# Performance work log

Hardware: AMD Instinct MI355X
Metric: run time of the kernel (lower is better)

## Reference

```python
import jax, jax.numpy as jnp
import numpy as np

INPUT_SIZE = 2048
HIDDEN_SIZE = 2048
BATCH = 4096


def setup_inputs() -> dict:
    key = jax.random.key(0)
    ks = jax.random.split(key, 24)
    s_in = 1.0 / np.sqrt(INPUT_SIZE)
    s_h = 1.0 / np.sqrt(HIDDEN_SIZE)
    inp = {
        "x": jax.random.normal(ks[0], (BATCH, INPUT_SIZE), jnp.float32),
        "h_prev": jax.random.normal(ks[1], (BATCH, HIDDEN_SIZE), jnp.float32),
        "c_prev": jax.random.normal(ks[2], (BATCH, HIDDEN_SIZE), jnp.float32),
        "n_prev": jnp.ones((BATCH, HIDDEN_SIZE), jnp.float32),
        "m_prev": jnp.zeros((BATCH, HIDDEN_SIZE), jnp.float32),
    }
    # 4 input projections (W*x) and 4 recurrent projections (R*h), each Linear w/ bias.
    names_x = ["Wzx", "Wix", "Wfx", "Wox"]
    names_h = ["Rzh", "Rih", "Rfh", "Roh"]
    for j, n in enumerate(names_x):
        inp[n + "_w"] = jax.random.uniform(ks[3 + 2 * j], (HIDDEN_SIZE, INPUT_SIZE), jnp.float32, -s_in, s_in)
        inp[n + "_b"] = jax.random.uniform(ks[4 + 2 * j], (HIDDEN_SIZE,), jnp.float32, -s_in, s_in)
    for j, n in enumerate(names_h):
        inp[n + "_w"] = jax.random.uniform(ks[11 + 2 * j], (HIDDEN_SIZE, HIDDEN_SIZE), jnp.float32, -s_h, s_h)
        inp[n + "_b"] = jax.random.uniform(ks[12 + 2 * j], (HIDDEN_SIZE,), jnp.float32, -s_h, s_h)
    return inp


def _lin(x, w, b):
    return x @ w.T + b


def reference(x, h_prev, c_prev, n_prev, m_prev,
              Wzx_w, Wzx_b, Wix_w, Wix_b, Wfx_w, Wfx_b, Wox_w, Wox_b,
              Rzh_w, Rzh_b, Rih_w, Rih_b, Rfh_w, Rfh_b, Roh_w, Roh_b):
    z = jnp.tanh(_lin(x, Wzx_w, Wzx_b) + _lin(h_prev, Rzh_w, Rzh_b))
    # log(i) and log(f) are the pre-activations (i = exp(pre_i), f = exp(pre_f))
    log_i = _lin(x, Wix_w, Wix_b) + _lin(h_prev, Rih_w, Rih_b)
    log_f = _lin(x, Wfx_w, Wfx_b) + _lin(h_prev, Rfh_w, Rfh_b)
    o = jax.nn.sigmoid(_lin(x, Wox_w, Wox_b) + _lin(h_prev, Roh_w, Roh_b))
    m = jnp.maximum(log_f + m_prev, log_i)  # stabilizer state
    i_hat = jnp.exp(log_i - m)
    f_hat = jnp.exp(log_f + m_prev - m)
    c = f_hat * c_prev + i_hat * z
    n = f_hat * n_prev + i_hat
    h = o * c / n
    return (h, c, n, m)
```

## Files before the change

kernel.cpp:

```cpp
#include <hip/hip_runtime.h>
#include <hip/hip_bf16.h>


#define BATCH 4096
#define NHID  2048
#define KDIM  4096
#define NTOT  8388608L
#define AW_OFS 16777216

typedef float  f32x4   __attribute__((ext_vector_type(4)));
typedef short  short8  __attribute__((ext_vector_type(8)));
typedef unsigned short ushort8 __attribute__((ext_vector_type(8)));

#define GL_LDS16(gp, lp)                                                      \
    __builtin_amdgcn_global_load_lds(                                         \
        (const __attribute__((address_space(1))) void*)(gp),                  \
        (__attribute__((address_space(3))) void*)(lp), 16, 0, 0)

__device__ __forceinline__ unsigned short f2bf(float f) {
    unsigned u = __float_as_uint(f);
    unsigned r = (u + 0x7fffu + ((u >> 16) & 1u)) >> 16;
    return (unsigned short)r;
}

__global__ void convA_kernel(const float* __restrict__ x,
                             const float* __restrict__ h,
                             unsigned short* __restrict__ A) {
    int gid = blockIdx.x * 256 + threadIdx.x;
    int row = gid >> 9;
    int col = (gid & 511) << 3;
    const float* src = (col < 2048) ? (x + (long)row * 2048 + col)
                                    : (h + (long)row * 2048 + (col - 2048));
    f32x4 v0 = __builtin_nontemporal_load((const f32x4*)src);
    f32x4 v1 = __builtin_nontemporal_load((const f32x4*)src + 1);
    ushort8 o;
    o[0] = f2bf(v0[0]); o[1] = f2bf(v0[1]); o[2] = f2bf(v0[2]); o[3] = f2bf(v0[3]);
    o[4] = f2bf(v1[0]); o[5] = f2bf(v1[1]); o[6] = f2bf(v1[2]); o[7] = f2bf(v1[3]);
    *(ushort8*)(A + ((long)row << 12) + col) = o;
}

__global__ void convW_kernel(const float* __restrict__ w0, const float* __restrict__ w1,
                             const float* __restrict__ w2, const float* __restrict__ w3,
                             const float* __restrict__ w4, const float* __restrict__ w5,
                             const float* __restrict__ w6, const float* __restrict__ w7,
                             unsigned short* __restrict__ Wb) {
    int z = blockIdx.y;
    const float* src;
    switch (z) {
        case 0: src = w0; break; case 1: src = w1; break;
        case 2: src = w2; break; case 3: src = w3; break;
        case 4: src = w4; break; case 5: src = w5; break;
        case 6: src = w6; break; default: src = w7; break;
    }
    int gid = blockIdx.x * 256 + threadIdx.x;
    int row = gid >> 8;
    int col = (gid & 255) << 3;
    const float* p = src + (long)row * 2048 + col;
    f32x4 v0 = __builtin_nontemporal_load((const f32x4*)p);
    f32x4 v1 = __builtin_nontemporal_load((const f32x4*)p + 1);
    ushort8 o;
    o[0] = f2bf(v0[0]); o[1] = f2bf(v0[1]); o[2] = f2bf(v0[2]); o[3] = f2bf(v0[3]);
    o[4] = f2bf(v1[0]); o[5] = f2bf(v1[1]); o[6] = f2bf(v1[2]); o[7] = f2bf(v1[3]);
    int g = z & 3, hf = z >> 2;
    *(ushort8*)(Wb + (long)g * NHID * KDIM + (long)row * KDIM + hf * 2048 + col) = o;
}

__global__ void bias_kernel(const float* __restrict__ b0, const float* __restrict__ b1,
                            const float* __restrict__ b2, const float* __restrict__ b3,
                            const float* __restrict__ r0, const float* __restrict__ r1,
                            const float* __restrict__ r2, const float* __restrict__ r3,
                            float* __restrict__ Bb) {
    int gid = blockIdx.x * 256 + threadIdx.x;
    int g = gid >> 11, j = gid & 2047;
    const float *wb, *rb;
    switch (g) {
        case 0: wb = b0; rb = r0; break; case 1: wb = b1; rb = r1; break;
        case 2: wb = b2; rb = r2; break; default: wb = b3; rb = r3; break;
    }
    Bb[gid] = wb[j] + rb[j];
}

__global__ __launch_bounds__(512, 4) void slstm_kernel(
    const __hip_bfloat16* __restrict__ A,
    const float* __restrict__ Bb,
    const float* __restrict__ c_prev,
    const float* __restrict__ n_prev,
    const float* __restrict__ m_prev,
    float* __restrict__ out)
{
    __shared__ uint4 smem4[49152 / 16];
    char* smem = (char*)smem4;

    const int tid  = threadIdx.x;
    const int lane = tid & 63;
    const int wv   = tid >> 6;
    const int gate = wv & 3;
    const int rh   = wv >> 2;
    const int lm   = lane & 15;
    const int quad = lane >> 4;
    const int l7   = lm & 7;

    const int row0 = blockIdx.x * 128;
    const int col0 = blockIdx.y * 64;

    int gofs[6]; char* lds[6];
#pragma unroll
    for (int t = 0; t < 6; ++t) {
        int id = wv * 6 + t;
        if (id < 16) {
            int idx = id * 64 + lane;
            int r = idx >> 3, jj = idx & 7;
            int j = jj ^ (r & 7);
            gofs[t] = (row0 + r) * KDIM + j * 8;
            lds[t]  = smem + id * 1024;
        } else {
            int idx = (id - 16) * 64 + lane;
            int g = idx >> 9, rr = (idx >> 3) & 63, jj = idx & 7;
            int j = jj ^ (rr & 7);
            gofs[t] = AW_OFS + (g * NHID + col0 + rr) * KDIM + j * 8;
            lds[t]  = smem + 16384 + (id - 16) * 1024;
        }
    }

    f32x4 acc[4][4];
#pragma unroll
    for (int mt = 0; mt < 4; ++mt)
#pragma unroll
        for (int nt = 0; nt < 4; ++nt)
#pragma unroll
            for (int r = 0; r < 4; ++r) acc[mt][nt][r] = 0.0f;

    const char* aB = smem + rh * 8192;
    const char* bB = smem + 16384 + gate * 8192;

    for (int kt = 0; kt < KDIM / 64; ++kt) {
        const int k0 = kt * 64;
        __syncthreads();
#pragma unroll
        for (int t = 0; t < 6; ++t) GL_LDS16(A + gofs[t] + k0, lds[t]);
        __syncthreads();
#pragma unroll
        for (int kk = 0; kk < 2; ++kk) {
            const int cof = ((kk * 4 + quad) ^ l7) * 16;
            short8 af[4], bf[4];
#pragma unroll
            for (int mt = 0; mt < 4; ++mt)
                af[mt] = *(const short8*)(aB + (mt * 16 + lm) * 128 + cof);
#pragma unroll
            for (int nt = 0; nt < 4; ++nt)
                bf[nt] = *(const short8*)(bB + (nt * 16 + lm) * 128 + cof);
#pragma unroll
            for (int mt = 0; mt < 4; ++mt)
#pragma unroll
                for (int nt = 0; nt < 4; ++nt)
                    acc[mt][nt] = __builtin_amdgcn_mfma_f32_16x16x32_bf16(
                        af[mt], bf[nt], acc[mt][nt], 0, 0, 0);
        }
    }

    float* exch = (float*)smem;
#pragma unroll
    for (int mt = 0; mt < 4; ++mt) {
        __syncthreads();
#pragma unroll
        for (int nt = 0; nt < 4; ++nt)
#pragma unroll
            for (int r = 0; r < 4; ++r)
                exch[((rh * 4 + gate) * 16 + quad * 4 + r) * 65 + nt * 16 + lm] =
                    acc[mt][nt][r];
        __syncthreads();
#pragma unroll
        for (int q = 0; q < 4; ++q) {
            int e   = q * 512 + tid;
            int erh = e >> 10, row = (e >> 6) & 15, col = e & 63;
            int R = row0 + erh * 64 + mt * 16 + row;
            int C = col0 + col;
            long idx = (long)R * NHID + C;
            float zp = exch[((erh * 4 + 0) * 16 + row) * 65 + col] + Bb[C];
            float ip = exch[((erh * 4 + 1) * 16 + row) * 65 + col] + Bb[2048 + C];
            float fp = exch[((erh * 4 + 2) * 16 + row) * 65 + col] + Bb[4096 + C];
            float op = exch[((erh * 4 + 3) * 16 + row) * 65 + col] + Bb[6144 + C];
            float cp = __builtin_nontemporal_load(c_prev + idx);
            float np = __builtin_nontemporal_load(n_prev + idx);
            float mp = __builtin_nontemporal_load(m_prev + idx);
            float z  = tanhf(zp);
            float o  = 1.0f / (1.0f + __expf(-op));
            float mm = fmaxf(fp + mp, ip);
            float ih = __expf(ip - mm);
            float fh = __expf(fp + mp - mm);
            float cc = fh * cp + ih * z;
            float nn = fh * np + ih;
            float hh = o * cc / nn;
            __builtin_nontemporal_store(hh, out + idx);
            __builtin_nontemporal_store(cc, out + NTOT + idx);
            __builtin_nontemporal_store(nn, out + 2 * NTOT + idx);
            __builtin_nontemporal_store(mm, out + 3 * NTOT + idx);
        }
    }
}

extern "C" void kernel_launch(void* const* d_in, const int* in_sizes, int n_in,
                              void* d_out, int out_size, void* d_ws, size_t ws_size,
                              hipStream_t stream) {
    const float* x      = (const float*)d_in[0];
    const float* h_prev = (const float*)d_in[1];
    const float* c_prev = (const float*)d_in[2];
    const float* n_prev = (const float*)d_in[3];
    const float* m_prev = (const float*)d_in[4];
    unsigned short* A  = (unsigned short*)d_ws;
    unsigned short* Wb = (unsigned short*)((char*)d_ws + 33554432);
    float*          Bb = (float*)((char*)d_ws + 100663296);

    convA_kernel<<<8192, 256, 0, stream>>>(x, h_prev, A);
    convW_kernel<<<dim3(2048, 8), 256, 0, stream>>>(
        (const float*)d_in[5], (const float*)d_in[7], (const float*)d_in[9],
        (const float*)d_in[11], (const float*)d_in[13], (const float*)d_in[15],
        (const float*)d_in[17], (const float*)d_in[19], Wb);
    bias_kernel<<<32, 256, 0, stream>>>(
        (const float*)d_in[6], (const float*)d_in[8], (const float*)d_in[10],
        (const float*)d_in[12], (const float*)d_in[14], (const float*)d_in[16],
        (const float*)d_in[18], (const float*)d_in[20], Bb);

    slstm_kernel<<<dim3(32, 32), 512, 0, stream>>>(
        (const __hip_bfloat16*)A, Bb, c_prev, n_prev, m_prev, (float*)d_out);
}
```

Before: 583.9 us.

## Pre-pack operands into k-chunk-major layout and switch to 32x32x16 MFMA

The conversion kernels now stage through shared memory and write A and W in a k-chunk-major packed layout (8 bf16 per chunk, rows contiguous). The GEMM loads straight from that layout into LDS without XOR swizzling and uses 32x32x16 bf16 MFMA with a 2x2 accumulator tile per wave instead of 4x4 16x16 tiles. It also raises wave priority around the MFMA section. The aim is to cut LDS read instructions and address arithmetic per MFMA. The unswizzled LDS layout may add bank conflicts, and the transpose adds an extra sync to the conversion kernels.

```diff
diff --git a/kernel.cpp b/kernel.cpp
--- a/kernel.cpp
+++ b/kernel.cpp
@@ -9,6 +9,7 @@
 #define AW_OFS 16777216
 
 typedef float  f32x4   __attribute__((ext_vector_type(4)));
+typedef float  f32x16  __attribute__((ext_vector_type(16)));
 typedef short  short8  __attribute__((ext_vector_type(8)));
 typedef unsigned short ushort8 __attribute__((ext_vector_type(8)));
 
@@ -25,26 +26,35 @@
 
 __global__ void convA_kernel(const float* __restrict__ x,
                              const float* __restrict__ h,
-                             unsigned short* __restrict__ A) {
-    int gid = blockIdx.x * 256 + threadIdx.x;
-    int row = gid >> 9;
-    int col = (gid & 511) << 3;
-    const float* src = (col < 2048) ? (x + (long)row * 2048 + col)
-                                    : (h + (long)row * 2048 + (col - 2048));
+                             unsigned short* __restrict__ Ap) {
+    __shared__ unsigned short tile[8][32][8];
+    const int t  = threadIdx.x;
+    const int r  = t >> 3, c8 = t & 7;
+    const int row = blockIdx.x * 32 + r;
+    const int k0  = blockIdx.y * 64;
+    const float* src = (blockIdx.y < 32)
+        ? (x + (long)row * 2048 + k0 + c8 * 8)
+        : (h + (long)row * 2048 + (k0 - 2048) + c8 * 8);
     f32x4 v0 = __builtin_nontemporal_load((const f32x4*)src);
     f32x4 v1 = __builtin_nontemporal_load((const f32x4*)src + 1);
     ushort8 o;
     o[0] = f2bf(v0[0]); o[1] = f2bf(v0[1]); o[2] = f2bf(v0[2]); o[3] = f2bf(v0[3]);
     o[4] = f2bf(v1[0]); o[5] = f2bf(v1[1]); o[6] = f2bf(v1[2]); o[7] = f2bf(v1[3]);
-    *(ushort8*)(A + ((long)row << 12) + col) = o;
+    *(ushort8*)&tile[c8][(r ^ (c8 << 2)) & 31][0] = o;
+    __syncthreads();
+    const int kcl = t >> 5, rr = t & 31;
+    ushort8 w = *(ushort8*)&tile[kcl][(rr ^ (kcl << 2)) & 31][0];
+    long dst = ((long)(blockIdx.y * 8 + kcl) * 4096 + blockIdx.x * 32 + rr) * 8;
+    __builtin_nontemporal_store(w, (ushort8*)(Ap + dst));
 }
 
 __global__ void convW_kernel(const float* __restrict__ w0, const float* __restrict__ w1,
                              const float* __restrict__ w2, const float* __restrict__ w3,
                              const float* __restrict__ w4, const float* __restrict__ w5,
                              const float* __restrict__ w6, const float* __restrict__ w7,
-                             unsigned short* __restrict__ Wb) {
-    int z = blockIdx.y;
+                             unsigned short* __restrict__ Wp) {
+    __shared__ unsigned short tile[8][32][8];
+    const int z = blockIdx.z;
     const float* src;
     switch (z) {
         case 0: src = w0; break; case 1: src = w1; break;
@@ -52,17 +62,24 @@
         case 4: src = w4; break; case 5: src = w5; break;
         case 6: src = w6; break; default: src = w7; break;
     }
-    int gid = blockIdx.x * 256 + threadIdx.x;
-    int row = gid >> 8;
-    int col = (gid & 255) << 3;
-    const float* p = src + (long)row * 2048 + col;
+    const int g = z & 3, hf = z >> 2;
+    const int t = threadIdx.x;
+    const int r = t >> 3, c8 = t & 7;
+    const int j  = blockIdx.x * 32 + r;
+    const int k2 = blockIdx.y * 64 + c8 * 8;
+    const float* p = src + (long)j * 2048 + k2;
     f32x4 v0 = __builtin_nontemporal_load((const f32x4*)p);
     f32x4 v1 = __builtin_nontemporal_load((const f32x4*)p + 1);
     ushort8 o;
     o[0] = f2bf(v0[0]); o[1] = f2bf(v0[1]); o[2] = f2bf(v0[2]); o[3] = f2bf(v0[3]);
     o[4] = f2bf(v1[0]); o[5] = f2bf(v1[1]); o[6] = f2bf(v1[2]); o[7] = f2bf(v1[3]);
-    int g = z & 3, hf = z >> 2;
-    *(ushort8*)(Wb + (long)g * NHID * KDIM + (long)row * KDIM + hf * 2048 + col) = o;
+    *(ushort8*)&tile[c8][(r ^ (c8 << 2)) & 31][0] = o;
+    __syncthreads();
+    const int kcl = t >> 5, rr = t & 31;
+    ushort8 w = *(ushort8*)&tile[kcl][(rr ^ (kcl << 2)) & 31][0];
+    const int kcg = hf * 256 + blockIdx.y * 8 + kcl;
+    long dst = ((long)kcg * 8192 + g * 2048 + blockIdx.x * 32 + rr) * 8;
+    __builtin_nontemporal_store(w, (ushort8*)(Wp + dst));
 }
 
 __global__ void bias_kernel(const float* __restrict__ b0, const float* __restrict__ b1,
@@ -81,7 +98,7 @@
 }
 
 __global__ __launch_bounds__(512, 4) void slstm_kernel(
-    const __hip_bfloat16* __restrict__ A,
+    const unsigned short* __restrict__ Ap,
     const float* __restrict__ Bb,
     const float* __restrict__ c_prev,
     const float* __restrict__ n_prev,
@@ -96,90 +113,90 @@
     const int wv   = tid >> 6;
     const int gate = wv & 3;
     const int rh   = wv >> 2;
-    const int lm   = lane & 15;
-    const int quad = lane >> 4;
-    const int l7   = lm & 7;
+    const int l31  = lane & 31;
+    const int lhi  = lane >> 5;
 
     const int row0 = blockIdx.x * 128;
     const int col0 = blockIdx.y * 64;
 
-    int gofs[6]; char* lds[6];
+    const int abase = lhi * 2048 + (rh * 64 + l31) * 16;
+    const int bbase = 16384 + lhi * 4096 + (gate * 64 + l31) * 16;
+
+    int gofs[6], strd[6], lofs[6];
 #pragma unroll
     for (int t = 0; t < 6; ++t) {
         int id = wv * 6 + t;
+        lofs[t] = id * 1024 + lane * 16;
         if (id < 16) {
             int idx = id * 64 + lane;
-            int r = idx >> 3, jj = idx & 7;
-            int j = jj ^ (r & 7);
-            gofs[t] = (row0 + r) * KDIM + j * 8;
-            lds[t]  = smem + id * 1024;
+            int kc = idx >> 7, row = idx & 127;
+            gofs[t] = (kc * 4096 + row0 + row) * 8;
+            strd[t] = 8 * 4096 * 8;
         } else {
             int idx = (id - 16) * 64 + lane;
-            int g = idx >> 9, rr = (idx >> 3) & 63, jj = idx & 7;
-            int j = jj ^ (rr & 7);
-            gofs[t] = AW_OFS + (g * NHID + col0 + rr) * KDIM + j * 8;
-            lds[t]  = smem + 16384 + (id - 16) * 1024;
-        }
-    }
-
-    f32x4 acc[4][4];
-#pragma unroll
-    for (int mt = 0; mt < 4; ++mt)
-#pragma unroll
-        for (int nt = 0; nt < 4; ++nt)
-#pragma unroll
-            for (int r = 0; r < 4; ++r) acc[mt][nt][r] = 0.0f;
-
-    const char* aB = smem + rh * 8192;
-    const char* bB = smem + 16384 + gate * 8192;
-
-    for (int kt = 0; kt < KDIM / 64; ++kt) {
-        const int k0 = kt * 64;
-        __syncthreads();
-#pragma unroll
-        for (int t = 0; t < 6; ++t) GL_LDS16(A + gofs[t] + k0, lds[t]);
-        __syncthreads();
-#pragma unroll
-        for (int kk = 0; kk < 2; ++kk) {
-            const int cof = ((kk * 4 + quad) ^ l7) * 16;
-            short8 af[4], bf[4];
-#pragma unroll
-            for (int mt = 0; mt < 4; ++mt)
-                af[mt] = *(const short8*)(aB + (mt * 16 + lm) * 128 + cof);
-#pragma unroll
-            for (int nt = 0; nt < 4; ++nt)
-                bf[nt] = *(const short8*)(bB + (nt * 16 + lm) * 128 + cof);
-#pragma unroll
-            for (int mt = 0; mt < 4; ++mt)
-#pragma unroll
-                for (int nt = 0; nt < 4; ++nt)
-                    acc[mt][nt] = __builtin_amdgcn_mfma_f32_16x16x32_bf16(
-                        af[mt], bf[nt], acc[mt][nt], 0, 0, 0);
-        }
+            int kc = idx >> 8, gr = idx & 255;
+            gofs[t] = AW_OFS + (kc * 8192 + (gr >> 6) * 2048 + col0 + (gr & 63)) * 8;
+            strd[t] = 8 * 8192 * 8;
+        }
+    }
+
+    f32x16 acc[2][2];
+#pragma unroll
+    for (int mt = 0; mt < 2; ++mt)
+#pragma unroll
+        for (int nt = 0; nt < 2; ++nt)
+#pragma unroll
+            for (int r = 0; r < 16; ++r) acc[mt][nt][r] = 0.0f;
+
+    for (int kt = 0; kt < 64; ++kt) {
+        __syncthreads();
+#pragma unroll
+        for (int t = 0; t < 6; ++t) {
+            GL_LDS16(Ap + gofs[t], smem + lofs[t]);
+            gofs[t] += strd[t];
+        }
+        __syncthreads();
+
+        __builtin_amdgcn_s_setprio(1);
+#pragma unroll
+        for (int ks = 0; ks < 4; ++ks) {
+            short8 a0 = *(const short8*)(smem + abase + ks * 4096);
+            short8 a1 = *(const short8*)(smem + abase + ks * 4096 + 512);
+            short8 b0 = *(const short8*)(smem + bbase + ks * 8192);
+            short8 b1 = *(const short8*)(smem + bbase + ks * 8192 + 512);
+            acc[0][0] = __builtin_amdgcn_mfma_f32_32x32x16_bf16(a0, b0, acc[0][0], 0, 0, 0);
+            acc[0][1] = __builtin_amdgcn_mfma_f32_32x32x16_bf16(a0, b1, acc[0][1], 0, 0, 0);
+            acc[1][0] = __builtin_amdgcn_mfma_f32_32x32x16_bf16(a1, b0, acc[1][0], 0, 0, 0);
+            acc[1][1] = __builtin_amdgcn_mfma_f32_32x32x16_bf16(a1, b1, acc[1][1], 0, 0, 0);
+        }
+        __builtin_amdgcn_s_setprio(0);
     }
 
     float* exch = (float*)smem;
 #pragma unroll
-    for (int mt = 0; mt < 4; ++mt) {
-        __syncthreads();
-#pragma unroll
-        for (int nt = 0; nt < 4; ++nt)
-#pragma unroll
-            for (int r = 0; r < 4; ++r)
-                exch[((rh * 4 + gate) * 16 + quad * 4 + r) * 65 + nt * 16 + lm] =
-                    acc[mt][nt][r];
+    for (int s = 0; s < 4; ++s) {
+        __syncthreads();
+        if (rh == (s >> 1)) {
+#pragma unroll
+            for (int nt = 0; nt < 2; ++nt)
+#pragma unroll
+                for (int r = 0; r < 16; ++r) {
+                    int lrow = (r & 3) + 8 * (r >> 2) + 4 * lhi;
+                    exch[(gate * 32 + lrow) * 65 + nt * 32 + l31] = acc[s & 1][nt][r];
+                }
+        }
         __syncthreads();
 #pragma unroll
         for (int q = 0; q < 4; ++q) {
             int e   = q * 512 + tid;
-            int erh = e >> 10, row = (e >> 6) & 15, col = e & 63;
-            int R = row0 + erh * 64 + mt * 16 + row;
+            int row = e >> 6, col = e & 63;
+            int R = row0 + s * 32 + row;
             int C = col0 + col;
             long idx = (long)R * NHID + C;
-            float zp = exch[((erh * 4 + 0) * 16 + row) * 65 + col] + Bb[C];
-            float ip = exch[((erh * 4 + 1) * 16 + row) * 65 + col] + Bb[2048 + C];
-            float fp = exch[((erh * 4 + 2) * 16 + row) * 65 + col] + Bb[4096 + C];
-            float op = exch[((erh * 4 + 3) * 16 + row) * 65 + col] + Bb[6144 + C];
+            float zp = exch[(0 * 32 + row) * 65 + col] + Bb[C];
+            float ip = exch[(1 * 32 + row) * 65 + col] + Bb[2048 + C];
+            float fp = exch[(2 * 32 + row) * 65 + col] + Bb[4096 + C];
+            float op = exch[(3 * 32 + row) * 65 + col] + Bb[6144 + C];
             float cp = __builtin_nontemporal_load(c_prev + idx);
             float np = __builtin_nontemporal_load(n_prev + idx);
             float mp = __builtin_nontemporal_load(m_prev + idx);
@@ -207,20 +224,20 @@
     const float* c_prev = (const float*)d_in[2];
     const float* n_prev = (const float*)d_in[3];
     const float* m_prev = (const float*)d_in[4];
-    unsigned short* A  = (unsigned short*)d_ws;
-    unsigned short* Wb = (unsigned short*)((char*)d_ws + 33554432);
+    unsigned short* Ap = (unsigned short*)d_ws;
+    unsigned short* Wp = (unsigned short*)((char*)d_ws + 33554432);
     float*          Bb = (float*)((char*)d_ws + 100663296);
 
-    convA_kernel<<<8192, 256, 0, stream>>>(x, h_prev, A);
-    convW_kernel<<<dim3(2048, 8), 256, 0, stream>>>(
+    convA_kernel<<<dim3(128, 64), 256, 0, stream>>>(x, h_prev, Ap);
+    convW_kernel<<<dim3(64, 32, 8), 256, 0, stream>>>(
         (const float*)d_in[5], (const float*)d_in[7], (const float*)d_in[9],
         (const float*)d_in[11], (const float*)d_in[13], (const float*)d_in[15],
-        (const float*)d_in[17], (const float*)d_in[19], Wb);
+        (const float*)d_in[17], (const float*)d_in[19], Wp);
     bias_kernel<<<32, 256, 0, stream>>>(
         (const float*)d_in[6], (const float*)d_in[8], (const float*)d_in[10],
         (const float*)d_in[12], (const float*)d_in[14], (const float*)d_in[16],
         (const float*)d_in[18], (const float*)d_in[20], Bb);
 
     slstm_kernel<<<dim3(32, 32), 512, 0, stream>>>(
-        (const __hip_bfloat16*)A, Bb, c_prev, n_prev, m_prev, (float*)d_out);
-}
+        Ap, Bb, c_prev, n_prev, m_prev, (float*)d_out);
+}
```

Measured after the change: 623.8 us. 1.07x slower.

## Double-buffer LDS tiles with K=32 steps to overlap global loads with MFMA

Applied to the files above, without the earlier changes.

Replaces the single-buffered K=64 main loop with a two-buffer K=32 pipeline. The next tile's global-to-LDS loads are issued before the current tile's MFMAs, so memory latency is hidden behind compute. Each iteration needs one waitcnt plus barrier instead of two syncthreads. The swizzle is reworked for 64-byte rows. The trade-offs are twice as many iterations, each with less work per barrier, and a vmcnt(0) wait that fully drains loads every step.

```diff
diff --git a/kernel.cpp b/kernel.cpp
--- a/kernel.cpp
+++ b/kernel.cpp
@@ -7,6 +7,7 @@
 #define KDIM  4096
 #define NTOT  8388608L
 #define AW_OFS 16777216
+#define BUFSZ 24576
 
 typedef float  f32x4   __attribute__((ext_vector_type(4)));
 typedef short  short8  __attribute__((ext_vector_type(8)));
@@ -88,7 +89,7 @@
     const float* __restrict__ m_prev,
     float* __restrict__ out)
 {
-    __shared__ uint4 smem4[49152 / 16];
+    __shared__ uint4 smem4[(2 * BUFSZ) / 16];
     char* smem = (char*)smem4;
 
     const int tid  = threadIdx.x;
@@ -98,27 +99,31 @@
     const int rh   = wv >> 2;
     const int lm   = lane & 15;
     const int quad = lane >> 4;
-    const int l7   = lm & 7;
 
     const int row0 = blockIdx.x * 128;
     const int col0 = blockIdx.y * 64;
 
-    int gofs[6]; char* lds[6];
-#pragma unroll
-    for (int t = 0; t < 6; ++t) {
-        int id = wv * 6 + t;
-        if (id < 16) {
+    const int cof   = ((quad ^ (lm & 3))) * 16;
+    const int abase = (rh * 64 + lm) * 64 + cof;
+    const int bbase = 8192 + (gate * 64 + lm) * 64 + cof;
+
+    int gofs[3], lofs[3];
+#pragma unroll
+    for (int t = 0; t < 3; ++t) {
+        int id = wv * 3 + t;
+        if (id < 8) {
             int idx = id * 64 + lane;
-            int r = idx >> 3, jj = idx & 7;
-            int j = jj ^ (r & 7);
+            int r = idx >> 2, jj = idx & 3;
+            int j = jj ^ (r & 3);
             gofs[t] = (row0 + r) * KDIM + j * 8;
-            lds[t]  = smem + id * 1024;
+            lofs[t] = idx * 16;
         } else {
-            int idx = (id - 16) * 64 + lane;
-            int g = idx >> 9, rr = (idx >> 3) & 63, jj = idx & 7;
-            int j = jj ^ (rr & 7);
+            int idx = (id - 8) * 64 + lane;
+            int gr = idx >> 2, jj = idx & 3;
+            int g = gr >> 6, rr = gr & 63;
+            int j = jj ^ (gr & 3);
             gofs[t] = AW_OFS + (g * NHID + col0 + rr) * KDIM + j * 8;
-            lds[t]  = smem + 16384 + (id - 16) * 1024;
+            lofs[t] = 8192 + idx * 16;
         }
     }
 
@@ -130,32 +135,40 @@
 #pragma unroll
             for (int r = 0; r < 4; ++r) acc[mt][nt][r] = 0.0f;
 
-    const char* aB = smem + rh * 8192;
-    const char* bB = smem + 16384 + gate * 8192;
-
-    for (int kt = 0; kt < KDIM / 64; ++kt) {
-        const int k0 = kt * 64;
-        __syncthreads();
-#pragma unroll
-        for (int t = 0; t < 6; ++t) GL_LDS16(A + gofs[t] + k0, lds[t]);
-        __syncthreads();
-#pragma unroll
-        for (int kk = 0; kk < 2; ++kk) {
-            const int cof = ((kk * 4 + quad) ^ l7) * 16;
-            short8 af[4], bf[4];
-#pragma unroll
-            for (int mt = 0; mt < 4; ++mt)
-                af[mt] = *(const short8*)(aB + (mt * 16 + lm) * 128 + cof);
+#pragma unroll
+    for (int t = 0; t < 3; ++t) {
+        GL_LDS16(A + gofs[t], smem + lofs[t]);
+        gofs[t] += 32;
+    }
+
+    for (int kt = 0; kt < 128; ++kt) {
+        asm volatile("s_waitcnt vmcnt(0)" ::: "memory");
+        __builtin_amdgcn_s_barrier();
+
+        const char* cur = smem + (kt & 1) * BUFSZ;
+        char*       wrt = smem + ((kt & 1) ^ 1) * BUFSZ;
+
+        if (kt < 127) {
+#pragma unroll
+            for (int t = 0; t < 3; ++t) {
+                GL_LDS16(A + gofs[t], wrt + lofs[t]);
+                gofs[t] += 32;
+            }
+        }
+
+        short8 af[4], bf[4];
+#pragma unroll
+        for (int mt = 0; mt < 4; ++mt)
+            af[mt] = *(const short8*)(cur + abase + mt * 1024);
+#pragma unroll
+        for (int nt = 0; nt < 4; ++nt)
+            bf[nt] = *(const short8*)(cur + bbase + nt * 1024);
+#pragma unroll
+        for (int mt = 0; mt < 4; ++mt)
 #pragma unroll
             for (int nt = 0; nt < 4; ++nt)
-                bf[nt] = *(const short8*)(bB + (nt * 16 + lm) * 128 + cof);
-#pragma unroll
-            for (int mt = 0; mt < 4; ++mt)
-#pragma unroll
-                for (int nt = 0; nt < 4; ++nt)
-                    acc[mt][nt] = __builtin_amdgcn_mfma_f32_16x16x32_bf16(
-                        af[mt], bf[nt], acc[mt][nt], 0, 0, 0);
-        }
+                acc[mt][nt] = __builtin_amdgcn_mfma_f32_16x16x32_bf16(
+                    af[mt], bf[nt], acc[mt][nt], 0, 0, 0);
     }
 
     float* exch = (float*)smem;
```

Result: slower. 603.4 us (+3.3%).
